# Performance work log

Measured on AMD Instinct MI355X. Metric: run time of the kernel, lower is better.

The kernel has to match this reference:

```python
import jax, jax.numpy as jnp
import numpy as np

N = 50000
E = 1600000
IN, HID, OUT = 32, 64, 64

def setup_inputs() -> dict:
    key = jax.random.key(0)
    ks = jax.random.split(key, 10)
    x1 = jax.random.normal(ks[0], (N, IN), dtype=jnp.float32)
    x2 = jax.random.normal(ks[1], (N, IN), dtype=jnp.float32)
    ei1 = jax.random.randint(ks[2], (2, E), 0, N, dtype=jnp.int64)
    ei2 = jax.random.randint(ks[3], (2, E), 0, N, dtype=jnp.int64)
    s1 = 1.0 / np.sqrt(2 * IN)
    s2 = 1.0 / np.sqrt(2 * HID)
    W1 = jax.random.uniform(ks[4], (2 * IN, HID), jnp.float32, -s1, s1)
    b1 = jax.random.uniform(ks[5], (HID,), jnp.float32, -s1, s1)
    prelu_a = jnp.full((HID,), 0.25, dtype=jnp.float32)  # PReLU per-channel init
    W2 = jax.random.uniform(ks[6], (2 * HID, OUT), jnp.float32, -s2, s2)
    b2 = jax.random.uniform(ks[7], (OUT,), jnp.float32, -s2, s2)
    return {"x1": x1, "edge_index1": ei1, "x2": x2, "edge_index2": ei2,
            "W1": W1, "b1": b1, "prelu_a": prelu_a, "W2": W2, "b2": b2}

def _edge_conv(x, src, dst, W, b, n_nodes):
    # PyG EdgeConv: msg = MLP([x_i, x_j - x_i]), aggr = max over incoming edges
    xi = x[dst]                     # [E, d] target node feats
    xj = x[src]                     # [E, d] source node feats
    msg = jax.nn.relu(jnp.concatenate([xi, xj - xi], axis=-1) @ W + b)  # [E, out]
    agg = jax.ops.segment_max(msg, dst, num_segments=n_nodes)
    return jnp.where(jnp.isfinite(agg), agg, 0.0)  # nodes with no in-edges -> 0

def _prelu(x, a):
    return jnp.where(x >= 0, x, a * x)

def _embed(x, edge_index, W1, b1, prelu_a, W2, b2):
    src, dst = edge_index[0], edge_index[1]
    h = _prelu(_edge_conv(x, src, dst, W1, b1, x.shape[0]), prelu_a)
    return _edge_conv(h, src, dst, W2, b2, x.shape[0])

def reference(x1, edge_index1, x2, edge_index2, W1, b1, prelu_a, W2, b2):
    e1 = _embed(x1, edge_index1, W1, b1, prelu_a, W2, b2)
    e2 = _embed(x2, edge_index2, W1, b1, prelu_a, W2, b2)
    return (e1, e2)
```

## Files before the change

kernel.cpp:

```cpp
#include <hip/hip_runtime.h>
#include <hip/hip_fp16.h>


constexpr int HID   = 64;
constexpr int TILE  = 64;
constexpr int TSH   = 6;
constexpr int CAP   = 2560;
constexpr int MAXNB = 1024;
constexpr int EPT   = 16;
constexpr int CAPN  = 96;

typedef _Float16 half8 __attribute__((ext_vector_type(8)));
typedef float    f32x4 __attribute__((ext_vector_type(4)));

__device__ __forceinline__ unsigned int pkmax(unsigned int a, unsigned int b) {
    unsigned int d;
    asm("v_pk_max_f16 %0, %1, %2" : "=v"(d) : "v"(a), "v"(b));
    return d;
}
__device__ __forceinline__ unsigned short f2hbits(float f) {
    const __half h = __float2half_rn(f);
    return *reinterpret_cast<const unsigned short*>(&h);
}
__device__ __forceinline__ float h2f(unsigned int b16) {
    const unsigned short b = (unsigned short)b16;
    __half h;
    *reinterpret_cast<unsigned short*>(&h) = b;
    return __half2float(h);
}

struct G {
    const float* x;
    const int*   src;
    const int*   dst;
    int* bcnt;
    unsigned int* bin;
    float*          u;
    unsigned short* vk;
    _Float16*       h;
    float*          out;
};

__global__ __launch_bounds__(256) void prep_w_kernel(
    const float* __restrict__ W1, const float* __restrict__ W2,
    _Float16* __restrict__ Wc1, _Float16* __restrict__ Wc2,
    unsigned short* __restrict__ vkS0, unsigned short* __restrict__ vkS1, int N)
{
    const int i = blockIdx.x * 256 + threadIdx.x;
    if (i < 32 * 64) {
        const int k = i >> 6, c = i & 63;
        const float lo = W1[k * 64 + c], hi = W1[(32 + k) * 64 + c];
        Wc1[k * 128 + c]      = (_Float16)(lo - hi);
        Wc1[k * 128 + 64 + c] = (_Float16)hi;
    }
    const int j = i - 32 * 64;
    if (j >= 0 && j < 64 * 64) {
        const int k = j >> 6, c = j & 63;
        const float lo = W2[k * 64 + c], hi = W2[(64 + k) * 64 + c];
        Wc2[k * 128 + c]      = (_Float16)(lo - hi);
        Wc2[k * 128 + 64 + c] = (_Float16)hi;
    }
    const int q = i - (32 * 64 + 64 * 64);
    if (q >= 0 && q < 2 * HID) {
        if (q < HID) vkS0[(size_t)N * HID + q]       = 0xFC00u;
        else         vkS1[(size_t)N * HID + (q-HID)] = 0xFC00u;
    }
}

__global__ __launch_bounds__(256) void bin_gemm32_kernel(
    G g0, G g1, int E, int NB, int N,
    const _Float16* __restrict__ Wc, const float* __restrict__ bias, int bBlk)
{
    const G g = blockIdx.y ? g1 : g0;

    if ((int)blockIdx.x < bBlk) {
        __shared__ int lh[MAXNB];
        __shared__ int lb[MAXNB];
        for (int i = threadIdx.x; i < NB; i += 256) lh[i] = 0;
        __syncthreads();

        const int base = blockIdx.x * 256 * EPT;
        unsigned int rec[EPT];
        int bb[EPT];
        #pragma unroll
        for (int k = 0; k < EPT; ++k) {
            const int i = base + k * 256 + threadIdx.x;
            if (i < E) {
                const int d = g.dst[i];
                const int s = g.src[i];
                rec[k] = ((unsigned int)s << TSH) | (unsigned int)(d & (TILE - 1));
                bb[k]  = d >> TSH;
                atomicAdd(&lh[bb[k]], 1);
            } else bb[k] = -1;
        }
        __syncthreads();
        for (int t = threadIdx.x; t < NB; t += 256) {
            const int c = lh[t];
            lb[t] = c ? atomicAdd(&g.bcnt[t], c) : 0;
            lh[t] = 0;
        }
        __syncthreads();
        #pragma unroll
        for (int k = 0; k < EPT; ++k) {
            if (bb[k] >= 0) {
                const int off = atomicAdd(&lh[bb[k]], 1);
                const int pos = lb[bb[k]] + off;
                if (pos < CAP)
                    g.bin[(size_t)bb[k] * CAP + pos] = rec[k];
            }
        }
        return;
    }

    constexpr int K = 32;
    const int lane = threadIdx.x & 63;
    const int m    = lane & 15;
    const int quad = lane >> 4;
    const int bx   = blockIdx.x - bBlk;
    const int wid  = (bx * 256 + threadIdx.x) >> 6;
    const int nW   = ((gridDim.x - bBlk) * 256) >> 6;

    half8 bf[8];
    #pragma unroll
    for (int t = 0; t < 8; ++t)
        #pragma unroll
        for (int j = 0; j < 8; ++j)
            bf[t][j] = Wc[(quad * 8 + j) * 128 + t * 16 + m];

    float bv[4];
    #pragma unroll
    for (int t = 0; t < 4; ++t) bv[t] = bias[t * 16 + m];

    const int tiles = (N + 15) / 16;
    for (int tile = wid; tile < tiles; tile += nW) {
        const int nbase = tile * 16;
        const int nodeA = min(nbase + m, N - 1);
        const float4* rp = (const float4*)(g.x + (size_t)nodeA * K);

        half8 a;
        {
            const float4 f0 = rp[quad * 2];
            const float4 f1 = rp[quad * 2 + 1];
            a[0] = (_Float16)f0.x; a[1] = (_Float16)f0.y;
            a[2] = (_Float16)f0.z; a[3] = (_Float16)f0.w;
            a[4] = (_Float16)f1.x; a[5] = (_Float16)f1.y;
            a[6] = (_Float16)f1.z; a[7] = (_Float16)f1.w;
        }

        f32x4 acc[8];
        #pragma unroll
        for (int t = 0; t < 8; ++t) {
            acc[t] = (f32x4){0.f, 0.f, 0.f, 0.f};
            acc[t] = __builtin_amdgcn_mfma_f32_16x16x32_f16(
                a, bf[t], acc[t], 0, 0, 0);
        }

        #pragma unroll
        for (int r = 0; r < 4; ++r) {
            const int node = nbase + quad * 4 + r;
            if (node < N) {
                float* urow = g.u + (size_t)node * HID;
                #pragma unroll
                for (int t = 0; t < 4; ++t)
                    urow[t * 16 + m] = acc[t][r] + bv[t];
                const unsigned int e0 = f2hbits(acc[4][r]);
                const unsigned int e1 = f2hbits(acc[5][r]);
                const unsigned int e2 = f2hbits(acc[6][r]);
                const unsigned int e3 = f2hbits(acc[7][r]);
                uint2 pack;
                pack.x = (e1 << 16) | e0;
                pack.y = (e3 << 16) | e2;
                ((uint2*)(g.vk + (size_t)node * HID))[m] = pack;
            }
        }
    }
}

__global__ __launch_bounds__(256) void gemm64_kernel(
    G g0, G g1, const _Float16* __restrict__ Wc,
    const float* __restrict__ bias, int N)
{
    const G g = blockIdx.y ? g1 : g0;
    constexpr int K = 64, KH = 2;
    const int lane = threadIdx.x & 63;
    const int m    = lane & 15;
    const int quad = lane >> 4;
    const int wid  = (blockIdx.x * 256 + threadIdx.x) >> 6;
    const int nW   = (gridDim.x * 256) >> 6;

    half8 bf[8][KH];
    #pragma unroll
    for (int t = 0; t < 8; ++t)
        #pragma unroll
        for (int hh = 0; hh < KH; ++hh)
            #pragma unroll
            for (int j = 0; j < 8; ++j)
                bf[t][hh][j] = Wc[(hh * 32 + quad * 8 + j) * 128 + t * 16 + m];

    float bv[4];
    #pragma unroll
    for (int t = 0; t < 4; ++t) bv[t] = bias[t * 16 + m];

    const int tiles = (N + 15) / 16;
    for (int tile = wid; tile < tiles; tile += nW) {
        const int nbase = tile * 16;
        const int nodeA = min(nbase + m, N - 1);
        const half8* rp = (const half8*)(g.h + (size_t)nodeA * K);

        half8 a[KH];
        #pragma unroll
        for (int hh = 0; hh < KH; ++hh) a[hh] = rp[hh * 4 + quad];

        f32x4 acc[8];
        #pragma unroll
        for (int t = 0; t < 8; ++t) {
            acc[t] = (f32x4){0.f, 0.f, 0.f, 0.f};
            #pragma unroll
            for (int hh = 0; hh < KH; ++hh)
                acc[t] = __builtin_amdgcn_mfma_f32_16x16x32_f16(
                    a[hh], bf[t][hh], acc[t], 0, 0, 0);
        }

        #pragma unroll
        for (int r = 0; r < 4; ++r) {
            const int node = nbase + quad * 4 + r;
            if (node < N) {
                float* urow = g.u + (size_t)node * HID;
                #pragma unroll
                for (int t = 0; t < 4; ++t)
                    urow[t * 16 + m] = acc[t][r] + bv[t];
                const unsigned int e0 = f2hbits(acc[4][r]);
                const unsigned int e1 = f2hbits(acc[5][r]);
                const unsigned int e2 = f2hbits(acc[6][r]);
                const unsigned int e3 = f2hbits(acc[7][r]);
                uint2 pack;
                pack.x = (e1 << 16) | e0;
                pack.y = (e3 << 16) | e2;
                ((uint2*)(g.vk + (size_t)node * HID))[m] = pack;
            }
        }
    }
}

template<bool OUT16>
__global__ __launch_bounds__(256) void agg_kernel(G g0, G g1, int N, int NB, int two) {
    int b, gi;
    if (two) {
        const int bid = blockIdx.x;
        const int xcd = bid & 7;
        gi = xcd >> 2;
        b  = (bid >> 3) * 4 + (xcd & 3);
    } else { gi = 0; b = blockIdx.x; }
    if (b >= NB) return;
    const G g = gi ? g1 : g0;

    __shared__ int lcnt[TILE];
    __shared__ alignas(16) unsigned short lrec[TILE][CAPN];
    for (int i = threadIdx.x; i < TILE; i += 256) lcnt[i] = 0;
    __syncthreads();

    const int cnt = min(g.bcnt[b], CAP);
    const unsigned int* __restrict__ bp = g.bin + (size_t)b * CAP;
    for (int i = threadIdx.x; i < cnt; i += 256) {
        const unsigned int rec = bp[i];
        const int d = rec & (TILE - 1);
        const int p = atomicAdd(&lcnt[d], 1);
        if (p < CAPN) lrec[d][p] = (unsigned short)(rec >> TSH);
    }
    __syncthreads();
    for (int t = threadIdx.x; t < TILE; t += 256) {
        const int c  = min(lcnt[t], CAPN);
        const int cp = (c + 7) & ~7;
        for (int p = c; p < cp; ++p) lrec[t][p] = (unsigned short)N;
        lcnt[t] = cp;
    }
    __syncthreads();

    const int grp = threadIdx.x >> 3;
    const int sub = threadIdx.x & 7;
    const uint4* __restrict__ vk4 = (const uint4*)g.vk;

    #pragma unroll
    for (int i = 0; i < 2; ++i) {
        const int nl = grp + 32 * i;
        const int n  = b * TILE + nl;
        if (n >= N) continue;
        const int cp = lcnt[nl];

        unsigned int m0 = 0xFC00FC00u, m1 = m0, m2 = m0, m3 = m0;
        for (int j = 0; j < cp; j += 8) {
            const uint4 rq = *(const uint4*)(&lrec[nl][j]);
            unsigned int s[8];
            s[0] = rq.x & 0xFFFFu; s[1] = rq.x >> 16;
            s[2] = rq.y & 0xFFFFu; s[3] = rq.y >> 16;
            s[4] = rq.z & 0xFFFFu; s[5] = rq.z >> 16;
            s[6] = rq.w & 0xFFFFu; s[7] = rq.w >> 16;
            uint4 a[8];
            #pragma unroll
            for (int k = 0; k < 8; ++k) a[k] = vk4[(size_t)s[k] * 8 + sub];
            #pragma unroll
            for (int k = 0; k < 8; ++k) {
                m0 = pkmax(m0, a[k].x);
                m1 = pkmax(m1, a[k].y);
                m2 = pkmax(m2, a[k].z);
                m3 = pkmax(m3, a[k].w);
            }
        }

        const bool has = cp > 0;
        const float2* __restrict__ u2 =
            (const float2*)(g.u + (size_t)n * HID);
        const float2 ua = u2[sub], ub = u2[sub + 8],
                     uc = u2[sub + 16], ud = u2[sub + 24];
        float r0, r1, r2, r3, r4, r5, r6, r7;
        r0 = has ? fmaxf(ua.x + h2f(m0 & 0xFFFFu), 0.f) : 0.f;
        r1 = has ? fmaxf(ua.y + h2f(m2 & 0xFFFFu), 0.f) : 0.f;
        r2 = has ? fmaxf(ub.x + h2f(m0 >> 16),     0.f) : 0.f;
        r3 = has ? fmaxf(ub.y + h2f(m2 >> 16),     0.f) : 0.f;
        r4 = has ? fmaxf(uc.x + h2f(m1 & 0xFFFFu), 0.f) : 0.f;
        r5 = has ? fmaxf(uc.y + h2f(m3 & 0xFFFFu), 0.f) : 0.f;
        r6 = has ? fmaxf(ud.x + h2f(m1 >> 16),     0.f) : 0.f;
        r7 = has ? fmaxf(ud.y + h2f(m3 >> 16),     0.f) : 0.f;
        if constexpr (OUT16) {
            unsigned int* hrow = (unsigned int*)(g.h + (size_t)n * HID);
            hrow[sub]      = (unsigned int)f2hbits(r0) | ((unsigned int)f2hbits(r1) << 16);
            hrow[sub + 8]  = (unsigned int)f2hbits(r2) | ((unsigned int)f2hbits(r3) << 16);
            hrow[sub + 16] = (unsigned int)f2hbits(r4) | ((unsigned int)f2hbits(r5) << 16);
            hrow[sub + 24] = (unsigned int)f2hbits(r6) | ((unsigned int)f2hbits(r7) << 16);
        } else {
            float2* orow = (float2*)(g.out + (size_t)n * HID);
            orow[sub]      = (float2){r0, r1};
            orow[sub + 8]  = (float2){r2, r3};
            orow[sub + 16] = (float2){r4, r5};
            orow[sub + 24] = (float2){r6, r7};
        }
    }
}


extern "C" void kernel_launch(void* const* d_in, const int* in_sizes, int n_in,
                              void* d_out, int out_size, void* d_ws, size_t ws_size,
                              hipStream_t stream) {
    const float* x1  = (const float*)d_in[0];
    const int*   ei1 = (const int*)d_in[1];
    const float* x2  = (const float*)d_in[2];
    const int*   ei2 = (const int*)d_in[3];
    const float* W1  = (const float*)d_in[4];
    const float* b1  = (const float*)d_in[5];
    const float* W2  = (const float*)d_in[7];
    const float* b2  = (const float*)d_in[8];

    const int N  = in_sizes[0] / 32;
    const int E  = in_sizes[1] / 2;
    const int NB = (N + TILE - 1) / TILE;
    float* out = (float*)d_out;

    const size_t rowB = (size_t)N * HID * sizeof(float);
    const size_t vkB  = ((size_t)(N + 1) * HID * 2 + 63) & ~(size_t)63;
    const size_t hB   = ((size_t)N * HID * 2 + 63) & ~(size_t)63;
    const size_t binB = ((size_t)NB * CAP * sizeof(int) + 63) & ~(size_t)63;
    const size_t nbB  = ((size_t)(NB + 2) * sizeof(int) + 63) & ~(size_t)63;
    const size_t wc1B = ((size_t)32 * 128 * 2 + 63) & ~(size_t)63;
    const size_t wc2B = ((size_t)64 * 128 * 2 + 63) & ~(size_t)63;

    const int bBlk = (E + 256 * EPT - 1) / (256 * EPT);
    const int gBlk = 512;
    const int pBlk = (32 * 64 + 64 * 64 + 2 * HID + 255) / 256;
    const int aggBlk2 = ((NB + 3) / 4) * 8;
    const int aggBlk1 = NB;

    _Float16* wc1 = nullptr;
    _Float16* wc2 = nullptr;

    auto run = [&](G ga, G gb, int ny) {
        hipMemsetAsync(ga.bcnt, 0, (size_t)ny * nbB, stream);
        bin_gemm32_kernel<<<dim3(bBlk + gBlk, ny), 256, 0, stream>>>(
            ga, gb, E, NB, N, wc1, b1, bBlk);
        if (ny == 2) agg_kernel<true><<<aggBlk2, 256, 0, stream>>>(ga, gb, N, NB, 1);
        else         agg_kernel<true><<<aggBlk1, 256, 0, stream>>>(ga, ga, N, NB, 0);
        gemm64_kernel<<<dim3(gBlk, ny), 256, 0, stream>>>(ga, gb, wc2, b2, N);
        if (ny == 2) agg_kernel<false><<<aggBlk2, 256, 0, stream>>>(ga, gb, N, NB, 1);
        else         agg_kernel<false><<<aggBlk1, 256, 0, stream>>>(ga, ga, N, NB, 0);
    };

    char* ws = (char*)d_ws;
    const size_t needBoth =
        2 * rowB + 2 * binB + 2 * vkB + 2 * hB + wc1B + wc2B + 2 * nbB;

    if (ws_size >= needBoth) {
        float* u0 = (float*)ws;                  ws += rowB;
        float* u1 = (float*)ws;                  ws += rowB;
        unsigned int* bin0 = (unsigned int*)ws;  ws += binB;
        unsigned int* bin1 = (unsigned int*)ws;  ws += binB;
        unsigned short* vk0 = (unsigned short*)ws;  ws += vkB;
        unsigned short* vk1 = (unsigned short*)ws;  ws += vkB;
        _Float16* h0 = (_Float16*)ws;            ws += hB;
        _Float16* h1 = (_Float16*)ws;            ws += hB;
        wc1 = (_Float16*)ws;                     ws += wc1B;
        wc2 = (_Float16*)ws;                     ws += wc2B;
        int* bcnt0 = (int*)ws;                   ws += nbB;
        int* bcnt1 = (int*)ws;

        G g0{x1, ei1, ei1 + E, bcnt0, bin0, u0, vk0, h0, out};
        G g1{x2, ei2, ei2 + E, bcnt1, bin1, u1, vk1, h1, out + (size_t)N * HID};
        prep_w_kernel<<<pBlk, 256, 0, stream>>>(W1, W2, wc1, wc2, vk0, vk1, N);
        run(g0, g1, 2);
    } else {
        float* u = (float*)ws;                   ws += rowB;
        unsigned int* bin = (unsigned int*)ws;   ws += binB;
        unsigned short* vk = (unsigned short*)ws;  ws += vkB;
        _Float16* h = (_Float16*)ws;             ws += hB;
        wc1 = (_Float16*)ws;                     ws += wc1B;
        wc2 = (_Float16*)ws;                     ws += wc2B;
        int* bcnt = (int*)ws;

        prep_w_kernel<<<pBlk, 256, 0, stream>>>(W1, W2, wc1, wc2, vk, vk, N);
        for (int g = 0; g < 2; ++g) {
            const int* ei = g ? ei2 : ei1;
            G gp{g ? x2 : x1, ei, ei + E, bcnt, bin,
                 u, vk, h, out + (size_t)g * N * HID};
            run(gp, gp, 1);
        }
    }
}
```

Measured before the change: 228.7 us.

## Stage binned edge records in LDS sorted by bucket before global scatter

The binning blocks now compute an exclusive prefix sum of per-bucket counts in shared memory, place each edge record into a locally bucket-sorted LDS array, and then write the records to global bins with consecutive threads. This turns random per-thread scatter stores into mostly contiguous runs per bucket, aiming to improve write coalescing. It adds about 24KB of LDS, an extra scan, and more barriers, which may reduce occupancy of the binning blocks.

```diff
diff --git a/kernel.cpp b/kernel.cpp
--- a/kernel.cpp
+++ b/kernel.cpp
@@ -75,8 +75,14 @@
 
     if ((int)blockIdx.x < bBlk) {
         __shared__ int lh[MAXNB];
-        __shared__ int lb[MAXNB];
-        for (int i = threadIdx.x; i < NB; i += 256) lh[i] = 0;
+        __shared__ int lof[MAXNB];
+        __shared__ int gbase[MAXNB];
+        __shared__ unsigned int   srec[256 * EPT];
+        __shared__ unsigned short sbkt[256 * EPT];
+        __shared__ int wsum[4];
+
+        const int tid = threadIdx.x;
+        for (int i = tid; i < NB; i += 256) lh[i] = 0;
         __syncthreads();
 
         const int base = blockIdx.x * 256 * EPT;
@@ -84,7 +90,7 @@
         int bb[EPT];
         #pragma unroll
         for (int k = 0; k < EPT; ++k) {
-            const int i = base + k * 256 + threadIdx.x;
+            const int i = base + k * 256 + tid;
             if (i < E) {
                 const int d = g.dst[i];
                 const int s = g.src[i];
@@ -94,20 +100,57 @@
             } else bb[k] = -1;
         }
         __syncthreads();
-        for (int t = threadIdx.x; t < NB; t += 256) {
-            const int c = lh[t];
-            lb[t] = c ? atomicAdd(&g.bcnt[t], c) : 0;
+
+        constexpr int CH = MAXNB / 256;
+        const int c0 = tid * CH;
+        int cl[CH], s = 0;
+        #pragma unroll
+        for (int c = 0; c < CH; ++c) {
+            cl[c] = (c0 + c < NB) ? lh[c0 + c] : 0;
+            s += cl[c];
+        }
+        const int lane = tid & 63, wv = tid >> 6;
+        int v = s;
+        #pragma unroll
+        for (int d = 1; d < 64; d <<= 1) {
+            const int t = __shfl_up(v, d);
+            if (lane >= d) v += t;
+        }
+        if (lane == 63) wsum[wv] = v;
+        __syncthreads();
+        int run = v - s;
+        for (int w = 0; w < wv; ++w) run += wsum[w];
+        #pragma unroll
+        for (int c = 0; c < CH; ++c) {
+            if (c0 + c < NB) lof[c0 + c] = run;
+            run += cl[c];
+        }
+        __syncthreads();
+
+        for (int t = tid; t < NB; t += 256) {
+            const int cc = lh[t];
+            const int rb = cc ? atomicAdd(&g.bcnt[t], cc) : 0;
+            gbase[t] = t * CAP + rb - lof[t];
             lh[t] = 0;
         }
         __syncthreads();
+
         #pragma unroll
         for (int k = 0; k < EPT; ++k) {
             if (bb[k] >= 0) {
-                const int off = atomicAdd(&lh[bb[k]], 1);
-                const int pos = lb[bb[k]] + off;
-                if (pos < CAP)
-                    g.bin[(size_t)bb[k] * CAP + pos] = rec[k];
+                const int p = lof[bb[k]] + atomicAdd(&lh[bb[k]], 1);
+                srec[p] = rec[k];
+                sbkt[p] = (unsigned short)bb[k];
             }
+        }
+        __syncthreads();
+
+        const int total = min(256 * EPT, E - base);
+        for (int i = tid; i < total; i += 256) {
+            const int bkt  = sbkt[i];
+            const int gidx = gbase[bkt] + i;
+            if (gidx < (bkt + 1) * CAP)
+                g.bin[gidx] = srec[i];
         }
         return;
     }
```

New measurement: 225.0 us. About the same (-1.6%).
